# Optimization experiments

Hardware: AMD Instinct MI355X
Metric: run time of the kernel (lower is better)

Reference implementation:

```python
import jax, jax.numpy as jnp
import numpy as np

N_NODES = 100000
N_EDGES = 1250000
E_FEAT = 64
IN_CH = 128
OUT_CH = 128


def setup_inputs() -> dict:
    key = jax.random.key(0)
    k1, k2, k3, k4, k5, k6, k7 = jax.random.split(key, 7)
    edge_index = jax.random.randint(k1, (2, N_EDGES), 0, N_NODES, dtype=jnp.int64 if jax.config.jax_enable_x64 else jnp.int32)
    edge_attr = jax.random.normal(k2, (N_EDGES, E_FEAT), dtype=jnp.float32)
    node_attr = jax.random.normal(k3, (N_NODES, IN_CH), dtype=jnp.float32)
    edge_weight = jax.random.uniform(k4, (N_EDGES,), dtype=jnp.float32)
    node_weight = jax.random.uniform(k5, (N_NODES,), dtype=jnp.float32)
    # Linear(in_channels + edge_features, out_channels): weight [out, in], bias [out]
    fan_in = IN_CH + E_FEAT
    bound = 1.0 / np.sqrt(fan_in)
    W = jax.random.uniform(k6, (OUT_CH, fan_in), minval=-bound, maxval=bound, dtype=jnp.float32)
    b = jax.random.uniform(k7, (OUT_CH,), minval=-bound, maxval=bound, dtype=jnp.float32)
    return {"edge_index": edge_index, "edge_attr": edge_attr, "node_attr": node_attr,
            "edge_weight": edge_weight, "node_weight": node_weight, "W": W, "b": b}


def reference(edge_index, edge_attr, node_attr, edge_weight, node_weight, W, b):
    num_nodes = node_attr.shape[0]  # original derives from edge_index.max()+1; static here for jit
    ea = edge_attr * edge_weight[:, None]                      # [E, F] weighted edge features
    tgt = edge_index[0]                                        # [E] target node per edge
    seg_sum = jax.ops.segment_sum(ea, tgt, num_segments=num_nodes)            # [N, F]
    cnt = jax.ops.segment_sum(jnp.ones((ea.shape[0],), ea.dtype), tgt, num_segments=num_nodes)  # [N]
    edge_mean = seg_sum / jnp.maximum(cnt, 1.0)[:, None]       # scatter_mean; zero-degree -> 0
    h = jnp.concatenate([node_attr, edge_mean], axis=1)        # [N, in+F]
    out = jax.nn.relu(h @ W.T + b)                             # [N, out]
    return out * node_weight[:, None]
```

## Files before the change

### kernel.cpp

```cpp
#include <hip/hip_runtime.h>


#define EF 64
#define IN_CH 128
#define OUT_CH 128
#define K_TOT 192

__global__ __launch_bounds__(256) void edge_scatter_kernel(
    const int* __restrict__ tgt,
    const float* __restrict__ edge_attr,
    const float* __restrict__ edge_weight,
    float* __restrict__ seg,
    float* __restrict__ cnt,
    int E)
{
    const int wave = (blockIdx.x * blockDim.x + threadIdx.x) >> 6;
    const int lane = threadIdx.x & 63;
    if (wave >= E) return;

    const int t = tgt[wave];
    const float ew = edge_weight[wave];
    const float v = edge_attr[(size_t)wave * EF + lane] * ew;

    atomicAdd(&seg[(size_t)t * EF + lane], v);
    if (lane == 0) atomicAdd(&cnt[t], 1.0f);
}

#define NB 64
#define KT 64
#define HP 68

__device__ __forceinline__ int wpos(int o) {
    return ((o >> 3) << 2) + (o & 3) + ((o & 4) ? 64 : 0);
}

__global__ __launch_bounds__(256) void node_gemm_kernel(
    const float* __restrict__ node_attr,
    const float* __restrict__ seg,
    const float* __restrict__ cnt,
    const float* __restrict__ W,
    const float* __restrict__ b,
    const float* __restrict__ node_weight,
    float* __restrict__ out,
    int N)
{
    __shared__ float W_lds[KT * OUT_CH];
    __shared__ float h_lds[KT * HP];

    const int tid   = threadIdx.x;
    const int node0 = blockIdx.x * NB;

    const int oc = tid & 15;
    const int o0 = oc * 8;
    const int n0 = (tid >> 4) * 4;

    const int s_node = tid >> 2;
    const int s_k0   = (tid & 3) * 16;
    const int w_o    = tid & 127;
    const int w_kh   = (tid >> 7) * 32;
    const int w_p    = wpos(w_o);

    float acc[4][8];
#pragma unroll
    for (int n = 0; n < 4; ++n)
#pragma unroll
        for (int j = 0; j < 8; ++j) acc[n][j] = 0.0f;

    const int gs_node = node0 + s_node;

    for (int kt = 0; kt < 3; ++kt) {
        const int k0 = kt * KT;
        __syncthreads();

        {
            const float* src = W + (size_t)w_o * K_TOT + k0 + w_kh;
#pragma unroll
            for (int i = 0; i < 32; i += 4) {
                const float4 wv = *reinterpret_cast<const float4*>(src + i);
                W_lds[(w_kh + i + 0) * OUT_CH + w_p] = wv.x;
                W_lds[(w_kh + i + 1) * OUT_CH + w_p] = wv.y;
                W_lds[(w_kh + i + 2) * OUT_CH + w_p] = wv.z;
                W_lds[(w_kh + i + 3) * OUT_CH + w_p] = wv.w;
            }
        }

        if (gs_node < N) {
            if (kt < 2) {
                const float* src = node_attr + (size_t)gs_node * IN_CH + k0 + s_k0;
#pragma unroll
                for (int i = 0; i < 16; i += 4) {
                    const float4 hv = *reinterpret_cast<const float4*>(src + i);
                    h_lds[(s_k0 + i + 0) * HP + s_node] = hv.x;
                    h_lds[(s_k0 + i + 1) * HP + s_node] = hv.y;
                    h_lds[(s_k0 + i + 2) * HP + s_node] = hv.z;
                    h_lds[(s_k0 + i + 3) * HP + s_node] = hv.w;
                }
            } else {
                const float inv = 1.0f / fmaxf(cnt[gs_node], 1.0f);
                const float* src = seg + (size_t)gs_node * EF + s_k0;
#pragma unroll
                for (int i = 0; i < 16; i += 4) {
                    const float4 sv = *reinterpret_cast<const float4*>(src + i);
                    h_lds[(s_k0 + i + 0) * HP + s_node] = sv.x * inv;
                    h_lds[(s_k0 + i + 1) * HP + s_node] = sv.y * inv;
                    h_lds[(s_k0 + i + 2) * HP + s_node] = sv.z * inv;
                    h_lds[(s_k0 + i + 3) * HP + s_node] = sv.w * inv;
                }
            }
        }
        __syncthreads();

#pragma unroll 4
        for (int k = 0; k < KT; ++k) {
            const float4 hv = *reinterpret_cast<const float4*>(&h_lds[k * HP + n0]);
            const float4 w0 = *reinterpret_cast<const float4*>(&W_lds[k * OUT_CH + oc * 4]);
            const float4 w1 = *reinterpret_cast<const float4*>(&W_lds[k * OUT_CH + 64 + oc * 4]);
            const float hh[4] = {hv.x, hv.y, hv.z, hv.w};
            const float ww[8] = {w0.x, w0.y, w0.z, w0.w, w1.x, w1.y, w1.z, w1.w};
#pragma unroll
            for (int n = 0; n < 4; ++n)
#pragma unroll
                for (int j = 0; j < 8; ++j)
                    acc[n][j] = fmaf(hh[n], ww[j], acc[n][j]);
        }
    }

    const float4 b0 = *reinterpret_cast<const float4*>(b + o0);
    const float4 b1 = *reinterpret_cast<const float4*>(b + o0 + 4);
    const float bb[8] = {b0.x, b0.y, b0.z, b0.w, b1.x, b1.y, b1.z, b1.w};

#pragma unroll
    for (int n = 0; n < 4; ++n) {
        const int gn = node0 + n0 + n;
        if (gn < N) {
            const float nw = node_weight[gn];
            float r[8];
#pragma unroll
            for (int j = 0; j < 8; ++j)
                r[j] = fmaxf(acc[n][j] + bb[j], 0.0f) * nw;
            float* dst = out + (size_t)gn * OUT_CH + o0;
            *reinterpret_cast<float4*>(dst)     = make_float4(r[0], r[1], r[2], r[3]);
            *reinterpret_cast<float4*>(dst + 4) = make_float4(r[4], r[5], r[6], r[7]);
        }
    }
}

extern "C" void kernel_launch(void* const* d_in, const int* in_sizes, int n_in,
                              void* d_out, int out_size, void* d_ws, size_t ws_size,
                              hipStream_t stream) {
    const int*   edge_index  = (const int*)d_in[0];
    const float* edge_attr   = (const float*)d_in[1];
    const float* node_attr   = (const float*)d_in[2];
    const float* edge_weight = (const float*)d_in[3];
    const float* node_weight = (const float*)d_in[4];
    const float* W           = (const float*)d_in[5];
    const float* b           = (const float*)d_in[6];
    float* out = (float*)d_out;

    const int E = in_sizes[0] / 2;
    const int N = in_sizes[2] / IN_CH;

    float* seg = (float*)d_ws;
    float* cnt = seg + (size_t)N * EF;
    const size_t zero_bytes = (size_t)N * EF * sizeof(float) + (size_t)N * sizeof(float);

    hipMemsetAsync(d_ws, 0, zero_bytes, stream);

    const int scatter_blocks = (E + 3) / 4;
    edge_scatter_kernel<<<scatter_blocks, 256, 0, stream>>>(
        edge_index, edge_attr, edge_weight, seg, cnt, E);

    const int gemm_blocks = (N + NB - 1) / NB;
    node_gemm_kernel<<<gemm_blocks, 256, 0, stream>>>(
        node_attr, seg, cnt, W, b, node_weight, out, N);
}
```

Measured before the change: 751.7 us.

## Replace float atomic scatter with CSR-style bucketing and per-node gather mean

```diff
diff --git a/kernel.cpp b/kernel.cpp
--- a/kernel.cpp
+++ b/kernel.cpp
@@ -6,24 +6,57 @@
 #define OUT_CH 128
 #define K_TOT 192
 
-__global__ __launch_bounds__(256) void edge_scatter_kernel(
-    const int* __restrict__ tgt,
+__global__ __launch_bounds__(256) void degree_kernel(
+    const int* __restrict__ tgt, int* __restrict__ deg, int E)
+{
+    const int e = blockIdx.x * blockDim.x + threadIdx.x;
+    if (e < E) atomicAdd(&deg[tgt[e]], 1);
+}
+
+__global__ __launch_bounds__(256) void assign_kernel(
+    const int* __restrict__ deg, int* __restrict__ cursor0,
+    int* __restrict__ base, int* __restrict__ cursor, int N)
+{
+    const int n = blockIdx.x * blockDim.x + threadIdx.x;
+    if (n < N) {
+        const int b = atomicAdd(cursor0, deg[n]);
+        base[n] = b;
+        cursor[n] = b;
+    }
+}
+
+__global__ __launch_bounds__(256) void reorder_kernel(
+    const int* __restrict__ tgt, int* __restrict__ cursor,
+    int* __restrict__ perm, int E)
+{
+    const int e = blockIdx.x * blockDim.x + threadIdx.x;
+    if (e < E) {
+        const int pos = atomicAdd(&cursor[tgt[e]], 1);
+        perm[pos] = e;
+    }
+}
+
+__global__ __launch_bounds__(256) void gather_mean_kernel(
     const float* __restrict__ edge_attr,
     const float* __restrict__ edge_weight,
-    float* __restrict__ seg,
-    float* __restrict__ cnt,
-    int E)
-{
-    const int wave = (blockIdx.x * blockDim.x + threadIdx.x) >> 6;
+    const int* __restrict__ perm,
+    const int* __restrict__ base,
+    const int* __restrict__ deg,
+    float* __restrict__ mean,
+    int N)
+{
+    const int n = (blockIdx.x * blockDim.x + threadIdx.x) >> 6;
     const int lane = threadIdx.x & 63;
-    if (wave >= E) return;
-
-    const int t = tgt[wave];
-    const float ew = edge_weight[wave];
-    const float v = edge_attr[(size_t)wave * EF + lane] * ew;
-
-    atomicAdd(&seg[(size_t)t * EF + lane], v);
-    if (lane == 0) atomicAdd(&cnt[t], 1.0f);
+    if (n >= N) return;
+
+    const int s = base[n];
+    const int d = deg[n];
+    float acc = 0.0f;
+    for (int i = 0; i < d; ++i) {
+        const int e = perm[s + i];
+        acc += edge_attr[(size_t)e * EF + lane] * edge_weight[e];
+    }
+    mean[(size_t)n * EF + lane] = acc / (float)max(d, 1);
 }
 
 #define NB 64
@@ -36,8 +69,7 @@
 
 __global__ __launch_bounds__(256) void node_gemm_kernel(
     const float* __restrict__ node_attr,
-    const float* __restrict__ seg,
-    const float* __restrict__ cnt,
+    const float* __restrict__ mean,
     const float* __restrict__ W,
     const float* __restrict__ b,
     const float* __restrict__ node_weight,
@@ -85,27 +117,16 @@
         }
 
         if (gs_node < N) {
-            if (kt < 2) {
-                const float* src = node_attr + (size_t)gs_node * IN_CH + k0 + s_k0;
-#pragma unroll
-                for (int i = 0; i < 16; i += 4) {
-                    const float4 hv = *reinterpret_cast<const float4*>(src + i);
-                    h_lds[(s_k0 + i + 0) * HP + s_node] = hv.x;
-                    h_lds[(s_k0 + i + 1) * HP + s_node] = hv.y;
-                    h_lds[(s_k0 + i + 2) * HP + s_node] = hv.z;
-                    h_lds[(s_k0 + i + 3) * HP + s_node] = hv.w;
-                }
-            } else {
-                const float inv = 1.0f / fmaxf(cnt[gs_node], 1.0f);
-                const float* src = seg + (size_t)gs_node * EF + s_k0;
-#pragma unroll
-                for (int i = 0; i < 16; i += 4) {
-                    const float4 sv = *reinterpret_cast<const float4*>(src + i);
-                    h_lds[(s_k0 + i + 0) * HP + s_node] = sv.x * inv;
-                    h_lds[(s_k0 + i + 1) * HP + s_node] = sv.y * inv;
-                    h_lds[(s_k0 + i + 2) * HP + s_node] = sv.z * inv;
-                    h_lds[(s_k0 + i + 3) * HP + s_node] = sv.w * inv;
-                }
+            const float* src = (kt < 2)
+                ? node_attr + (size_t)gs_node * IN_CH + k0 + s_k0
+                : mean      + (size_t)gs_node * EF   + s_k0;
+#pragma unroll
+            for (int i = 0; i < 16; i += 4) {
+                const float4 hv = *reinterpret_cast<const float4*>(src + i);
+                h_lds[(s_k0 + i + 0) * HP + s_node] = hv.x;
+                h_lds[(s_k0 + i + 1) * HP + s_node] = hv.y;
+                h_lds[(s_k0 + i + 2) * HP + s_node] = hv.z;
+                h_lds[(s_k0 + i + 3) * HP + s_node] = hv.w;
             }
         }
         __syncthreads();
@@ -160,17 +181,27 @@
     const int E = in_sizes[0] / 2;
     const int N = in_sizes[2] / IN_CH;
 
-    float* seg = (float*)d_ws;
-    float* cnt = seg + (size_t)N * EF;
-    const size_t zero_bytes = (size_t)N * EF * sizeof(float) + (size_t)N * sizeof(float);
-
-    hipMemsetAsync(d_ws, 0, zero_bytes, stream);
-
-    const int scatter_blocks = (E + 3) / 4;
-    edge_scatter_kernel<<<scatter_blocks, 256, 0, stream>>>(
-        edge_index, edge_attr, edge_weight, seg, cnt, E);
+    int*   deg     = (int*)d_ws;
+    int*   cursor0 = deg + N;
+    int*   base    = cursor0 + 1;
+    int*   cursor  = base + N;
+    int*   perm    = cursor + N;
+    float* mean    = (float*)(perm + E);
+
+    hipMemsetAsync(deg, 0, (size_t)(N + 1) * sizeof(int), stream);
+
+    const int eb = (E + 255) / 256;
+    const int nb = (N + 255) / 256;
+
+    degree_kernel <<<eb, 256, 0, stream>>>(edge_index, deg, E);
+    assign_kernel <<<nb, 256, 0, stream>>>(deg, cursor0, base, cursor, N);
+    reorder_kernel<<<eb, 256, 0, stream>>>(edge_index, cursor, perm, E);
+
+    const int gb = (N + 3) / 4;
+    gather_mean_kernel<<<gb, 256, 0, stream>>>(
+        edge_attr, edge_weight, perm, base, deg, mean, N);
 
     const int gemm_blocks = (N + NB - 1) / NB;
     node_gemm_kernel<<<gemm_blocks, 256, 0, stream>>>(
-        node_attr, seg, cnt, W, b, node_weight, out, N);
-}
+        node_attr, mean, W, b, node_weight, out, N);
+}
```

After: 824.7 us. 1.1x slower.
